# Kernel optimization log

Measured on AMD Instinct MI355X. Metric: run time of the kernel, lower is better.

Reference implementation:

```python
import jax, jax.numpy as jnp
import numpy as np

N = 16384       # input points
D_IN = 64       # feature dim
D_OUT = 128     # output dim
STRIDE = 4      # downsampling stride -> M = N // STRIDE sampled points
NSAMPLE = 16    # hard-coded in __init__
BN_EPS = 1e-5


def setup_inputs() -> dict:
    key = jax.random.key(0)
    k1, k2, k3 = jax.random.split(key, 3)
    p = jax.random.normal(k1, (N, 3), jnp.float32)
    x = jax.random.normal(k2, (N, D_IN), jnp.float32)
    o = jnp.array([N], jnp.int32)  # single-cloud offsets
    # mlp params: Linear(d_in+3, d_out) + BatchNorm1d(d_out)
    W = jax.random.normal(k3, (D_IN + 3, D_OUT), jnp.float32) * 0.05
    b = jnp.zeros((D_OUT,), jnp.float32)
    gamma = jnp.ones((D_OUT,), jnp.float32)
    beta = jnp.zeros((D_OUT,), jnp.float32)
    return {"p": p, "x": x, "o": o, "W": W, "b": b, "gamma": gamma, "beta": beta}


def fps(p, m):
    """Furthest point sampling: returns m indices into p [N,3]. Sequential by nature."""
    n = p.shape[0]
    dists = jnp.full((n,), jnp.inf, p.dtype)
    idxs = jnp.zeros((m,), jnp.int32)  # start from point 0 (pointops convention)

    def body(i, carry):
        idxs, dists = carry
        last = p[idxs[i - 1]]                      # [3]
        d = jnp.sum((p - last) ** 2, axis=1)       # [N]
        dists = jnp.minimum(dists, d)
        return idxs.at[i].set(jnp.argmax(dists).astype(jnp.int32)), dists

    idxs, _ = jax.lax.fori_loop(1, m, body, (idxs, dists))
    return idxs


def reference(p, x, o, W, b, gamma, beta):
    m = p.shape[0] // STRIDE  # static
    # --- furthest point sampling (non-differentiable index op, as in pointops) ---
    s_idx = fps(jax.lax.stop_gradient(p), m)
    n_p = p[s_idx]                                             # [M,3]
    # --- query-and-group: kNN of each sampled point over all N points ---
    d2 = (jnp.sum(n_p ** 2, axis=1)[:, None]
          + jnp.sum(p ** 2, axis=1)[None, :]
          - 2.0 * n_p @ p.T)                                   # [M,N]
    _, nn_idx = jax.lax.top_k(-d2, NSAMPLE)                    # [M,K]
    pj = p[nn_idx] - n_p[:, None, :]                           # [M,K,3] relative coords
    xj = x[nn_idx]                                             # [M,K,D_IN]
    # normalize relative coords by max neighbor norm per sampled point
    nrm = jnp.linalg.norm(pj, axis=-1, keepdims=True)          # [M,K,1]
    pj = pj / (jnp.max(nrm, axis=1, keepdims=True) + 1e-8)
    feat = jnp.concatenate([pj, xj], axis=-1).max(axis=1)      # [M, 3+D_IN] max-pool
    # --- MLP: Linear + BatchNorm1d (training stats) + ReLU ---
    h = feat @ W + b                                           # [M, D_OUT]
    mean = jnp.mean(h, axis=0)
    var = jnp.var(h, axis=0)
    h = (h - mean) / jnp.sqrt(var + BN_EPS) * gamma + beta
    x_out = jax.nn.relu(h)
    n_o = jnp.array([m], jnp.int32)
    return (n_p, x_out, n_o)
```

## Files before the change

kernel.cpp:

```cpp
#include <hip/hip_runtime.h>

#define N_PTS 16384
#define M_PTS 4096
#define D_INF 64
#define D_OUTF 128
#define KNN 16
#define DF 67

__global__ __launch_bounds__(256) void sp_kernel(const float* __restrict__ p,
                                                 float* __restrict__ spn) {
  int j = blockIdx.x * 256 + threadIdx.x;
  float a = p[3 * j], b = p[3 * j + 1], c = p[3 * j + 2];
  spn[j] = __fadd_rn(__fadd_rn(__fmul_rn(a, a), __fmul_rn(b, b)), __fmul_rn(c, c));
}

#define FPS_T 512
#define FPS_PPT 32

__global__ __launch_bounds__(FPS_T) void fps_kernel(const float* __restrict__ p,
                                                    int* __restrict__ sidx,
                                                    float* __restrict__ np_out) {
  const int t = threadIdx.x;
  float px[FPS_PPT], py[FPS_PPT], pz[FPS_PPT], dd[FPS_PPT];
#pragma unroll
  for (int k = 0; k < FPS_PPT; ++k) {
    int j = t + (k << 9);
    px[k] = p[3 * j]; py[k] = p[3 * j + 1]; pz[k] = p[3 * j + 2];
    dd[k] = INFINITY;
  }
  __shared__ float s_wmax[FPS_T / 64];
  __shared__ float s_last[3];
  __shared__ int s_widx;
  if (t == 0) {
    s_widx = 0x7FFFFFFF;
    s_last[0] = px[0]; s_last[1] = py[0]; s_last[2] = pz[0];
    sidx[0] = 0;
    np_out[0] = px[0]; np_out[1] = py[0]; np_out[2] = pz[0];
  }
  __syncthreads();
  for (int i = 1; i < M_PTS; ++i) {
    float lx = s_last[0], ly = s_last[1], lz = s_last[2];
    float tmax = -INFINITY;
#pragma unroll
    for (int k = 0; k < FPS_PPT; ++k) {
      float dx = __fsub_rn(px[k], lx);
      float dy = __fsub_rn(py[k], ly);
      float dz = __fsub_rn(pz[k], lz);
      float d = __fadd_rn(__fadd_rn(__fmul_rn(dx, dx), __fmul_rn(dy, dy)),
                          __fmul_rn(dz, dz));
      float nd = fminf(dd[k], d);
      dd[k] = nd;
      tmax = fmaxf(tmax, nd);
    }
    float wmax = tmax;
#pragma unroll
    for (int off = 32; off >= 1; off >>= 1)
      wmax = fmaxf(wmax, __shfl_xor(wmax, off));
    if ((t & 63) == 0) s_wmax[t >> 6] = wmax;
    __syncthreads();
    float gmax = s_wmax[0];
#pragma unroll
    for (int wv = 1; wv < FPS_T / 64; ++wv) gmax = fmaxf(gmax, s_wmax[wv]);
    int m = 0x7FFFFFFF;
    float cx = 0.f, cy = 0.f, cz = 0.f;
    if (tmax == gmax) {
#pragma unroll
      for (int k = FPS_PPT - 1; k >= 0; --k) {
        if (dd[k] == gmax) { m = t + (k << 9); cx = px[k]; cy = py[k]; cz = pz[k]; }
      }
      atomicMin(&s_widx, m);
    }
    __syncthreads();
    int widx = s_widx;
    if (m != 0x7FFFFFFF && m == widx) {
      s_last[0] = cx; s_last[1] = cy; s_last[2] = cz;
      s_widx = 0x7FFFFFFF;
      sidx[i] = m;
      np_out[3 * i] = cx; np_out[3 * i + 1] = cy; np_out[3 * i + 2] = cz;
    }
    __syncthreads();
  }
}

__global__ __launch_bounds__(256) void knn_feat_kernel(const float* __restrict__ p,
                                                       const float* __restrict__ x,
                                                       const float* __restrict__ spn,
                                                       const int* __restrict__ sidx,
                                                       float* __restrict__ feat) {
  __shared__ float cd[4][256];
  __shared__ int ci[4][256];
  __shared__ int cnt[4];
  __shared__ int s_nn[4][KNN];
  const int w = threadIdx.x >> 6;
  const int lane = threadIdx.x & 63;
  const int q = (blockIdx.x << 2) + w;
  const int qi = sidx[q];
  const float qx = p[3 * qi], qy = p[3 * qi + 1], qz = p[3 * qi + 2];
  const float sn = spn[qi];
  if (lane == 0) cnt[w] = 0;
  float lmin = INFINITY;
  for (int it = 0; it < N_PTS / 64; ++it) {
    int j = lane + (it << 6);
    float dot = __fmaf_rn(qz, p[3 * j + 2],
                 __fmaf_rn(qy, p[3 * j + 1], __fmul_rn(qx, p[3 * j])));
    float d2 = __fsub_rn(__fadd_rn(sn, spn[j]), __fmul_rn(2.0f, dot));
    lmin = fminf(lmin, d2);
  }
  float mv = lmin;
  float tau = INFINITY;
#pragma unroll
  for (int r = 0; r < KNN; ++r) {
    float rmin = mv;
#pragma unroll
    for (int off = 32; off >= 1; off >>= 1) rmin = fminf(rmin, __shfl_xor(rmin, off));
    tau = rmin;
    unsigned long long msk = __ballot(mv == rmin);
    if (lane == (int)(__ffsll(msk) - 1)) mv = INFINITY;
  }
  __syncthreads();
  for (int it = 0; it < N_PTS / 64; ++it) {
    int j = lane + (it << 6);
    float dot = __fmaf_rn(qz, p[3 * j + 2],
                 __fmaf_rn(qy, p[3 * j + 1], __fmul_rn(qx, p[3 * j])));
    float d2 = __fsub_rn(__fadd_rn(sn, spn[j]), __fmul_rn(2.0f, dot));
    if (d2 <= tau) {
      int pos = atomicAdd(&cnt[w], 1);
      if (pos < 256) { cd[w][pos] = d2; ci[w][pos] = j; }
    }
  }
  __syncthreads();
  int C = min(cnt[w], 256);
  float vv[4]; int ii[4];
#pragma unroll
  for (int s = 0; s < 4; ++s) {
    int pos = lane + (s << 6);
    bool ok = pos < C;
    vv[s] = ok ? cd[w][pos] : INFINITY;
    ii[s] = ok ? ci[w][pos] : 0x7FFFFFFF;
  }
#pragma unroll
  for (int r = 0; r < KNN; ++r) {
    float bv = vv[0]; int bi = ii[0]; int bs = 0;
#pragma unroll
    for (int s = 1; s < 4; ++s) {
      bool tk = (vv[s] < bv) || (vv[s] == bv && ii[s] < bi);
      bv = tk ? vv[s] : bv; bi = tk ? ii[s] : bi; bs = tk ? s : bs;
    }
    float rv = bv; int ri = bi;
#pragma unroll
    for (int off = 32; off >= 1; off >>= 1) {
      float ov = __shfl_xor(rv, off); int oi = __shfl_xor(ri, off);
      bool tk = (ov < rv) || (ov == rv && oi < ri);
      rv = tk ? ov : rv; ri = tk ? oi : ri;
    }
    if (bi == ri) {
#pragma unroll
      for (int s = 0; s < 4; ++s) if (s == bs) vv[s] = INFINITY;
    }
    if (lane == 0) s_nn[w][r] = ri;
  }
  __syncthreads();
  float ax = -INFINITY, ay = -INFINITY, az = -INFINITY, nr = -INFINITY;
  if (lane < KNN) {
    int jn = s_nn[w][lane];
    ax = __fsub_rn(p[3 * jn], qx);
    ay = __fsub_rn(p[3 * jn + 1], qy);
    az = __fsub_rn(p[3 * jn + 2], qz);
    nr = sqrtf(__fadd_rn(__fadd_rn(__fmul_rn(ax, ax), __fmul_rn(ay, ay)),
                         __fmul_rn(az, az)));
  }
  float mnr = nr, mx = ax, my = ay, mz = az;
#pragma unroll
  for (int off = 32; off >= 1; off >>= 1) {
    mnr = fmaxf(mnr, __shfl_xor(mnr, off));
    mx = fmaxf(mx, __shfl_xor(mx, off));
    my = fmaxf(my, __shfl_xor(my, off));
    mz = fmaxf(mz, __shfl_xor(mz, off));
  }
  if (lane == 0) {
    float sden = __fadd_rn(mnr, 1e-8f);
    feat[q * DF + 0] = mx / sden;
    feat[q * DF + 1] = my / sden;
    feat[q * DF + 2] = mz / sden;
  }
  float fm = -INFINITY;
#pragma unroll
  for (int k = 0; k < KNN; ++k) {
    int jn = s_nn[w][k];
    fm = fmaxf(fm, x[(jn << 6) + lane]);
  }
  feat[q * DF + 3 + lane] = fm;
}

__global__ __launch_bounds__(128) void mlp_kernel(const float* __restrict__ feat,
                                                  const float* __restrict__ W,
                                                  const float* __restrict__ b,
                                                  float* __restrict__ h) {
  int mrow = blockIdx.x;
  int o = threadIdx.x;
  const float* fr = feat + mrow * DF;
  float acc = b[o];
#pragma unroll
  for (int k = 0; k < DF; ++k) acc = __fmaf_rn(fr[k], W[k * D_OUTF + o], acc);
  h[mrow * D_OUTF + o] = acc;
}

__global__ __launch_bounds__(256) void stats_kernel(const float* __restrict__ h,
                                                    const float* __restrict__ gamma,
                                                    const float* __restrict__ beta,
                                                    float* __restrict__ scsh) {
  int o = blockIdx.x;
  int t = threadIdx.x;
  float s = 0.f, s2 = 0.f;
  for (int mrow = t; mrow < M_PTS; mrow += 256) {
    float v = h[mrow * D_OUTF + o];
    s += v;
    s2 = __fmaf_rn(v, v, s2);
  }
#pragma unroll
  for (int off = 32; off >= 1; off >>= 1) {
    s += __shfl_xor(s, off);
    s2 += __shfl_xor(s2, off);
  }
  __shared__ float as1[4], as2[4];
  if ((t & 63) == 0) { as1[t >> 6] = s; as2[t >> 6] = s2; }
  __syncthreads();
  if (t == 0) {
    float ts = ((as1[0] + as1[1]) + as1[2]) + as1[3];
    float ts2 = ((as2[0] + as2[1]) + as2[2]) + as2[3];
    float mean = ts / (float)M_PTS;
    float var = ts2 / (float)M_PTS - mean * mean;
    var = fmaxf(var, 0.f);
    float sc = gamma[o] / sqrtf(var + 1e-5f);
    scsh[o] = sc;
    scsh[D_OUTF + o] = beta[o] - mean * sc;
  }
}

__global__ __launch_bounds__(256) void bn_kernel(const float* __restrict__ h,
                                                 const float* __restrict__ scsh,
                                                 float* __restrict__ out) {
  int idx = blockIdx.x * 256 + threadIdx.x;
  int o = idx & (D_OUTF - 1);
  float v = __fmaf_rn(h[idx], scsh[o], scsh[D_OUTF + o]);
  out[M_PTS * 3 + idx] = fmaxf(v, 0.f);
  if (idx == 0) out[M_PTS * 3 + M_PTS * D_OUTF] = 4096.0f;
}

extern "C" void kernel_launch(void* const* d_in, const int* in_sizes, int n_in,
                              void* d_out, int out_size, void* d_ws, size_t ws_size,
                              hipStream_t stream) {
  const float* p     = (const float*)d_in[0];
  const float* x     = (const float*)d_in[1];
  const float* W     = (const float*)d_in[3];
  const float* b     = (const float*)d_in[4];
  const float* gamma = (const float*)d_in[5];
  const float* beta  = (const float*)d_in[6];
  float* out = (float*)d_out;

  float* wsf  = (float*)d_ws;
  int*   sidx = (int*)d_ws;
  float* spn  = wsf + 4096;
  float* feat = spn + N_PTS;
  float* h    = feat + M_PTS * DF;
  float* scsh = h + M_PTS * D_OUTF;

  sp_kernel<<<N_PTS / 256, 256, 0, stream>>>(p, spn);
  fps_kernel<<<1, FPS_T, 0, stream>>>(p, sidx, out);
  knn_feat_kernel<<<M_PTS / 4, 256, 0, stream>>>(p, x, spn, sidx, feat);
  mlp_kernel<<<M_PTS, D_OUTF, 0, stream>>>(feat, W, b, h);
  stats_kernel<<<D_OUTF, 256, 0, stream>>>(h, gamma, beta, scsh);
  bn_kernel<<<(M_PTS * D_OUTF) / 256, 256, 0, stream>>>(h, scsh, out);
}
```

Before: 7.278 ms.

## Use argmax shuffle reduction and double-buffered shared slots in FPS

Replaces the FPS per-iteration max reduce, atomicMin winner election and three barriers with a single (value,index) wave-shuffle argmax. Per-wave results go into parity-double-buffered shared arrays so only one __syncthreads is needed per iteration. Every thread reads the new last point from global memory instead of shared, and the launch bound adds a minimum of 2 blocks per CU, which may limit registers for the 128 per-thread point arrays. Fewer barriers shorten the sequential 4096-step loop, but each step now does a dependent global load.

```diff
diff --git a/kernel.cpp b/kernel.cpp
--- a/kernel.cpp
+++ b/kernel.cpp
@@ -17,9 +17,9 @@
 #define FPS_T 512
 #define FPS_PPT 32
 
-__global__ __launch_bounds__(FPS_T) void fps_kernel(const float* __restrict__ p,
-                                                    int* __restrict__ sidx,
-                                                    float* __restrict__ np_out) {
+__global__ __launch_bounds__(FPS_T, 2) void fps_kernel(const float* __restrict__ p,
+                                                       int* __restrict__ sidx,
+                                                       float* __restrict__ np_out) {
   const int t = threadIdx.x;
   float px[FPS_PPT], py[FPS_PPT], pz[FPS_PPT], dd[FPS_PPT];
 #pragma unroll
@@ -28,18 +28,14 @@
     px[k] = p[3 * j]; py[k] = p[3 * j + 1]; pz[k] = p[3 * j + 2];
     dd[k] = INFINITY;
   }
-  __shared__ float s_wmax[FPS_T / 64];
-  __shared__ float s_last[3];
-  __shared__ int s_widx;
+  __shared__ float s_v[2][FPS_T / 64];
+  __shared__ int   s_i[2][FPS_T / 64];
   if (t == 0) {
-    s_widx = 0x7FFFFFFF;
-    s_last[0] = px[0]; s_last[1] = py[0]; s_last[2] = pz[0];
     sidx[0] = 0;
-    np_out[0] = px[0]; np_out[1] = py[0]; np_out[2] = pz[0];
-  }
-  __syncthreads();
+    np_out[0] = p[0]; np_out[1] = p[1]; np_out[2] = p[2];
+  }
+  float lx = p[0], ly = p[1], lz = p[2];
   for (int i = 1; i < M_PTS; ++i) {
-    float lx = s_last[0], ly = s_last[1], lz = s_last[2];
     float tmax = -INFINITY;
 #pragma unroll
     for (int k = 0; k < FPS_PPT; ++k) {
@@ -52,33 +48,39 @@
       dd[k] = nd;
       tmax = fmaxf(tmax, nd);
     }
-    float wmax = tmax;
-#pragma unroll
-    for (int off = 32; off >= 1; off >>= 1)
-      wmax = fmaxf(wmax, __shfl_xor(wmax, off));
-    if ((t & 63) == 0) s_wmax[t >> 6] = wmax;
+    int bk = 0;
+#pragma unroll
+    for (int k = FPS_PPT - 1; k >= 0; --k) {
+      if (dd[k] == tmax) bk = k;
+    }
+    int ri = t + (bk << 9);
+    float rv = tmax;
+#pragma unroll
+    for (int off = 32; off >= 1; off >>= 1) {
+      float ov = __shfl_xor(rv, off);
+      int   oi = __shfl_xor(ri, off);
+      bool tk = (ov > rv) || (ov == rv && oi < ri);
+      rv = tk ? ov : rv;
+      ri = tk ? oi : ri;
+    }
+    const int par = i & 1;
+    if ((t & 63) == 0) { s_v[par][t >> 6] = rv; s_i[par][t >> 6] = ri; }
     __syncthreads();
-    float gmax = s_wmax[0];
-#pragma unroll
-    for (int wv = 1; wv < FPS_T / 64; ++wv) gmax = fmaxf(gmax, s_wmax[wv]);
-    int m = 0x7FFFFFFF;
-    float cx = 0.f, cy = 0.f, cz = 0.f;
-    if (tmax == gmax) {
-#pragma unroll
-      for (int k = FPS_PPT - 1; k >= 0; --k) {
-        if (dd[k] == gmax) { m = t + (k << 9); cx = px[k]; cy = py[k]; cz = pz[k]; }
-      }
-      atomicMin(&s_widx, m);
-    }
-    __syncthreads();
-    int widx = s_widx;
-    if (m != 0x7FFFFFFF && m == widx) {
-      s_last[0] = cx; s_last[1] = cy; s_last[2] = cz;
-      s_widx = 0x7FFFFFFF;
-      sidx[i] = m;
-      np_out[3 * i] = cx; np_out[3 * i + 1] = cy; np_out[3 * i + 2] = cz;
-    }
-    __syncthreads();
+    float gv = s_v[par][0];
+    int   gi = s_i[par][0];
+#pragma unroll
+    for (int w = 1; w < FPS_T / 64; ++w) {
+      float ov = s_v[par][w];
+      int   oi = s_i[par][w];
+      bool tk = (ov > gv) || (ov == gv && oi < gi);
+      gv = tk ? ov : gv;
+      gi = tk ? oi : gi;
+    }
+    lx = p[3 * gi]; ly = p[3 * gi + 1]; lz = p[3 * gi + 2];
+    if (t == 0) {
+      sidx[i] = gi;
+      np_out[3 * i] = lx; np_out[3 * i + 1] = ly; np_out[3 * i + 2] = lz;
+    }
   }
 }
 
```

Measured after the change: 8.623 ms. 1.18x slower.
